# Kernel tuning notes

Hardware: AMD Instinct MI355X
Metric: run time of the kernel (lower is better)

The kernel has to match this reference:

```python
import jax, jax.numpy as jnp
import numpy as np

EPS = 1e-7
TAU = 2.0  # curr_temp = max_temp at init
GROUPS = 2
NUM_CODES = 320


def setup_inputs() -> dict:
    key = jax.random.key(0)
    k1, k2, k3, k4 = jax.random.split(key, 4)
    B, T, C = 8, 2048, 1024
    GV = GROUPS * NUM_CODES  # 640
    D = 256
    x = jax.random.normal(k1, (B, T, C), dtype=jnp.float32)
    W = jax.random.normal(k2, (GV, C), dtype=jnp.float32)  # nn.init.normal_(std=1)
    b = jnp.zeros((GV,), dtype=jnp.float32)
    codebook = jax.random.uniform(k3, (1, GV, D), dtype=jnp.float32)  # uniform_ init
    u = jax.random.uniform(k4, (B * T * GROUPS, NUM_CODES), dtype=jnp.float32,
                           minval=1e-10, maxval=1.0)
    gumbel_noise = -jnp.log(-jnp.log(u))
    return {"x": x, "W": W, "b": b, "codebook": codebook, "gumbel_noise": gumbel_noise}


def reference(x, W, b, codebook, gumbel_noise):
    B, T, C = x.shape
    N = B * T
    G, V = GROUPS, NUM_CODES
    D = codebook.shape[-1]

    # weight projection -> logits [N, G*V]
    logits = jnp.einsum('nc,vc->nv', x.reshape(N, C), W) + b
    l = logits.reshape(N * G, V)

    # hard codes (no-grad path in torch)
    k = jnp.argmax(l, axis=-1)
    hard_x = jax.nn.one_hot(k, V, dtype=l.dtype).reshape(N, G, V)
    hard_probs = jax.lax.stop_gradient(hard_x).mean(axis=0)  # [G, V]
    code_perplexity = jnp.exp(-jnp.sum(hard_probs * jnp.log(hard_probs + EPS), axis=-1)).sum()

    avg_probs = jax.nn.softmax(l.reshape(N, G, V), axis=-1).mean(axis=0)  # [G, V]
    prob_perplexity = jnp.exp(-jnp.sum(avg_probs * jnp.log(avg_probs + EPS), axis=-1)).sum()

    # gumbel-softmax, hard=True with straight-through (training path)
    y_soft = jax.nn.softmax((l + gumbel_noise) / TAU, axis=-1)  # [N*G, V]
    idx = jnp.argmax(y_soft, axis=-1)
    y_hard = jax.nn.one_hot(idx, V, dtype=y_soft.dtype)
    y = y_hard + y_soft - jax.lax.stop_gradient(y_soft)

    # combine with codebook: (onehot-ish weights) @ codebook per group
    q = jnp.einsum('ngv,gvd->ngd', y.reshape(N, G, V), codebook.reshape(G, V, D))
    q = q.reshape(B, T, G * D)

    num_vars = G * V
    diversity_loss = (num_vars - prob_perplexity) / num_vars
    return q, code_perplexity, prob_perplexity, diversity_loss
```

## Files before the change

kernel.cpp:

```cpp
#include <hip/hip_runtime.h>

#define N_ROWS 16384
#define C_DIM  1024
#define GV     640
#define V_DIM  320
#define G_DIM  2
#define D_DIM  256
#define MROWS  64
#define FBLKS  (N_ROWS / MROWS)
#define NBUCKET 64

typedef __attribute__((ext_vector_type(8))) _Float16 half8;
typedef __attribute__((ext_vector_type(4))) _Float16 half4v;
typedef __attribute__((ext_vector_type(4))) float float4v;

#define LDS_AS(p) ((__attribute__((address_space(3))) unsigned int*)(p))
#define GLB_AS(p) ((const __attribute__((address_space(1))) unsigned int*)(p))

__global__ __launch_bounds__(256) void wsplit_kernel(const float* __restrict__ src,
                                                     _Float16* __restrict__ dst,
                                                     int* __restrict__ zr) {
  const int t = blockIdx.x * 256 + threadIdx.x;
  zr[t] = 0;
  const int n = t % GV;
  const int cc = t / GV;
  const int k = cc * 8;
  const float4 v0 = *(const float4*)(src + (size_t)n * C_DIM + k);
  const float4 v1 = *(const float4*)(src + (size_t)n * C_DIM + k + 4);
  half8 h;
  h[0] = (_Float16)v0.x; h[1] = (_Float16)v0.y; h[2] = (_Float16)v0.z; h[3] = (_Float16)v0.w;
  h[4] = (_Float16)v1.x; h[5] = (_Float16)v1.y; h[6] = (_Float16)v1.z; h[7] = (_Float16)v1.w;
  *(half8*)(dst + (size_t)t * 8) = h;
}

__global__ __launch_bounds__(512, 2) void fused_kernel(
    const float* __restrict__ x,
    const _Float16* __restrict__ whT,
    const float* __restrict__ bias,
    const float* __restrict__ gn,
    const float* __restrict__ cb,
    float* __restrict__ q,
    float* __restrict__ mf,
    int* __restrict__ mi) {
  __shared__ __align__(16) char smemU[98304];
  _Float16* BhL = (_Float16*)smemU;
  _Float16* AhL = (_Float16*)(smemU + 81920);
  _Float16* AlL = (_Float16*)(smemU + 90112);
  float* combW  = (float*)smemU;
  float* wbL    = (float*)(smemU + 18432);
  __shared__ float accL[GV];
  __shared__ int   cntL[GV];

  const int tid = threadIdx.x;
  const int lane = tid & 63;
  const int w = tid >> 6;
  const int m0 = blockIdx.x * MROWS;
  const int frow = lane & 15;
  const int quad = lane >> 4;

  for (int e = tid; e < GV; e += 512) { accL[e] = 0.0f; cntL[e] = 0; }

  const int ar = tid >> 3;
  const int ak = (tid & 7) * 4;
  const int ac = ak >> 3;
  const int ah_off = ak & 7;
  const float* xp = x + (size_t)(m0 + ar) * C_DIM + ak;

  float4v acc[4][5];
#pragma unroll
  for (int i = 0; i < 4; ++i)
#pragma unroll
    for (int j = 0; j < 5; ++j) acc[i][j] = (float4v)0.0f;

  auto stageB = [&](int kb, _Float16* Bh) {
    const _Float16* bsrc = whT + (size_t)kb * 2560 * 8;
#pragma unroll
    for (int s = 0; s < 5; ++s) {
      const int c = s * 512 + tid;
      __builtin_amdgcn_global_load_lds(GLB_AS(bsrc + (size_t)c * 8),
                                       LDS_AS(Bh + c * 8), 16, 0, 0);
    }
  };
  auto splitA = [&](const float4& a4, _Float16* Ah, _Float16* Al) {
    const _Float16 h0 = (_Float16)a4.x, h1 = (_Float16)a4.y;
    const _Float16 h2 = (_Float16)a4.z, h3 = (_Float16)a4.w;
    half4v hv, lv;
    hv[0] = h0; hv[1] = h1; hv[2] = h2; hv[3] = h3;
    lv[0] = (_Float16)(a4.x - (float)h0);
    lv[1] = (_Float16)(a4.y - (float)h1);
    lv[2] = (_Float16)(a4.z - (float)h2);
    lv[3] = (_Float16)(a4.w - (float)h3);
    *(half4v*)&Ah[(ac * 64 + ar) * 8 + ah_off] = hv;
    *(half4v*)&Al[(ac * 64 + ar) * 8 + ah_off] = lv;
  };

  float4 a4 = *(const float4*)xp;
  stageB(0, BhL);
  splitA(a4, AhL, AlL);
  a4 = *(const float4*)(xp + 32);
  __syncthreads();

  for (int kb = 0; kb < 32; ++kb) {
    const int cur = kb & 1;
    _Float16* BhC = BhL + cur * 20480;
    _Float16* AhC = AhL + cur * 2048;
    _Float16* AlC = AlL + cur * 2048;

    if (kb < 31) {
      const int nxt = cur ^ 1;
      stageB(kb + 1, BhL + nxt * 20480);
      splitA(a4, AhL + nxt * 2048, AlL + nxt * 2048);
      if (kb < 30) a4 = *(const float4*)(xp + (kb + 2) * 32);
    }

    half8 ah[4], al[4];
#pragma unroll
    for (int i = 0; i < 4; ++i) {
      ah[i] = *(const half8*)&AhC[(quad * 64 + 16 * i + frow) * 8];
      al[i] = *(const half8*)&AlC[(quad * 64 + 16 * i + frow) * 8];
    }
#pragma unroll
    for (int j = 0; j < 5; ++j) {
      const half8 bh = *(const half8*)&BhC[(quad * 640 + 80 * w + 16 * j + frow) * 8];
#pragma unroll
      for (int i = 0; i < 4; ++i) {
        acc[i][j] = __builtin_amdgcn_mfma_f32_16x16x32_f16(ah[i], bh, acc[i][j], 0, 0, 0);
        acc[i][j] = __builtin_amdgcn_mfma_f32_16x16x32_f16(al[i], bh, acc[i][j], 0, 0, 0);
      }
    }
    __syncthreads();
  }

  float bw[5];
#pragma unroll
  for (int j = 0; j < 5; ++j) bw[j] = bias[80 * w + 16 * j + frow];

  const int g  = w >> 2;
  const int wq = w & 3;

  float mlk[4][4];
#pragma unroll
  for (int i = 0; i < 4; ++i) {
#pragma unroll
    for (int r = 0; r < 4; ++r) {
      const int row = 16 * i + 4 * quad + r;
      const int n = m0 + row;
      const float* gp = gn + (size_t)(2 * n + g) * V_DIM + 80 * wq + frow;

      float l5[5], t5[5];
#pragma unroll
      for (int j = 0; j < 5; ++j) {
        l5[j] = acc[i][j][r] + bw[j];
        t5[j] = (l5[j] + gp[16 * j]) * 0.5f;
      }
      float ml = l5[0]; int il = 80 * wq + frow;
      float mt = t5[0]; int it = il;
#pragma unroll
      for (int j = 1; j < 5; ++j) {
        const int cj = 80 * wq + 16 * j + frow;
        if (l5[j] > ml) { ml = l5[j]; il = cj; }
        if (t5[j] > mt) { mt = t5[j]; it = cj; }
      }
#pragma unroll
      for (int off = 1; off < 16; off <<= 1) {
        const float o1 = __shfl_xor(ml, off, 64); const int i1 = __shfl_xor(il, off, 64);
        if (o1 > ml || (o1 == ml && i1 < il)) { ml = o1; il = i1; }
        const float o2 = __shfl_xor(mt, off, 64); const int i2 = __shfl_xor(it, off, 64);
        if (o2 > mt || (o2 == mt && i2 < it)) { mt = o2; it = i2; }
      }
      mlk[i][r] = ml;
      float sl = 0.0f, st = 0.0f;
#pragma unroll
      for (int j = 0; j < 5; ++j) {
        const float el = expf(l5[j] - ml);
        acc[i][j][r] = el;
        sl += el;
        st += expf(t5[j] - mt);
      }
#pragma unroll
      for (int off = 1; off < 16; off <<= 1) {
        sl += __shfl_xor(sl, off, 64);
        st += __shfl_xor(st, off, 64);
      }
      if (frow == 4 * i + r) {
        float* dst = combW + (size_t)(g * 64 + row) * 36 + wq * 8;
        float4v p1, p2;
        p1[0] = ml; p1[1] = __int_as_float(il); p1[2] = sl; p1[3] = 0.0f;
        p2[0] = mt; p2[1] = __int_as_float(it); p2[2] = st; p2[3] = 0.0f;
        *(float4v*)dst = p1;
        *(float4v*)(dst + 4) = p2;
      }
    }
  }
  __syncthreads();

  if (tid < 128) {
    const int rg = tid;
    const float* cw = combW + (size_t)rg * 36;
    float mw[4], sw[4], tw[4], s2[4];
    int   iw[4], ti4[4];
#pragma unroll
    for (int v = 0; v < 4; ++v) {
      const float4v p1 = *(const float4v*)(cw + v * 8);
      const float4v p2 = *(const float4v*)(cw + v * 8 + 4);
      mw[v] = p1[0]; iw[v] = __float_as_int(p1[1]); sw[v] = p1[2];
      tw[v] = p2[0]; ti4[v] = __float_as_int(p2[1]); s2[v] = p2[2];
    }
    float m = mw[0]; int idx = iw[0];
    float tm = tw[0]; int ti = ti4[0];
#pragma unroll
    for (int v = 1; v < 4; ++v) {
      if (mw[v] > m || (mw[v] == m && iw[v] < idx)) { m = mw[v]; idx = iw[v]; }
      if (tw[v] > tm || (tw[v] == tm && ti4[v] < ti)) { tm = tw[v]; ti = ti4[v]; }
    }
    float sl = 0.0f, st = 0.0f;
#pragma unroll
    for (int v = 0; v < 4; ++v) {
      sl += sw[v] * expf(mw[v] - m);
      st += s2[v] * expf(tw[v] - tm);
    }
    const float inv = 1.0f / sl;
    const float sv = 1.0f / st;
    const float yv = (1.0f + sv) - sv;
    const int g2 = rg >> 6;
    atomicAdd(&cntL[g2 * V_DIM + idx], 1);
    float4v wbv;
    wbv[0] = m; wbv[1] = inv; wbv[2] = yv; wbv[3] = __int_as_float(ti);
    *(float4v*)(wbL + (size_t)rg * 4) = wbv;
  }
  __syncthreads();

  float p5[5] = {0.0f, 0.0f, 0.0f, 0.0f, 0.0f};
#pragma unroll
  for (int i = 0; i < 4; ++i)
#pragma unroll
    for (int r = 0; r < 4; ++r) {
      const int row = 16 * i + 4 * quad + r;
      const float4v wbv = *(const float4v*)(wbL + (size_t)(g * 64 + row) * 4);
      const float k = expf(mlk[i][r] - wbv[0]) * wbv[1];
#pragma unroll
      for (int j = 0; j < 5; ++j) p5[j] += acc[i][j][r] * k;
    }
#pragma unroll
  for (int j = 0; j < 5; ++j)
    atomicAdd(&accL[g * V_DIM + 80 * wq + 16 * j + frow], p5[j]);

#pragma unroll
  for (int it2 = 0; it2 < 16; ++it2) {
    const int task = w + 8 * it2;
    const int tg = task >> 6, trow = task & 63;
    const float4v wbv = *(const float4v*)(wbL + (size_t)task * 4);
    const float yv = wbv[2];
    const int ti = __float_as_int(wbv[3]);
    const float4v c4 = ((const float4v*)cb)[(size_t)(tg * V_DIM + ti) * 64 + lane];
    float4v o4;
#pragma unroll
    for (int e2 = 0; e2 < 4; ++e2) o4[e2] = yv * c4[e2];
    ((float4v*)q)[(size_t)(m0 + trow) * 128 + tg * 64 + lane] = o4;
  }

  __syncthreads();
  const size_t pb = (size_t)(blockIdx.x & (NBUCKET - 1)) * GV;
  for (int e = tid; e < GV; e += 512) {
    atomicAdd(&mf[pb + e], accL[e]);
    atomicAdd(&mi[pb + e], cntL[e]);
  }
}

__global__ __launch_bounds__(640) void finalize_kernel(
    const float* __restrict__ mf, const int* __restrict__ mi,
    float* __restrict__ out3) {
  __shared__ float sA[G_DIM];
  __shared__ float sC[G_DIM];
  const int t = threadIdx.x;
  if (t < G_DIM) { sA[t] = 0.0f; sC[t] = 0.0f; }
  __syncthreads();

  const int g = t / V_DIM;
  float f = 0.0f;
  int   c = 0;
#pragma unroll 8
  for (int b = 0; b < NBUCKET; ++b) {
    f += mf[(size_t)b * GV + t];
    c += mi[(size_t)b * GV + t];
  }
  const float pa = f * (1.0f / 16384.0f);
  const float ph = (float)c * (1.0f / 16384.0f);
  float a = pa * logf(pa + 1e-7f);
  float h = ph * logf(ph + 1e-7f);
#pragma unroll
  for (int off = 32; off > 0; off >>= 1) {
    a += __shfl_xor(a, off, 64);
    h += __shfl_xor(h, off, 64);
  }
  if ((t & 63) == 0) {
    atomicAdd(&sA[g], a);
    atomicAdd(&sC[g], h);
  }
  __syncthreads();
  if (t == 0) {
    const float code_p = expf(-sC[0]) + expf(-sC[1]);
    const float prob_p = expf(-sA[0]) + expf(-sA[1]);
    out3[0] = code_p;
    out3[1] = prob_p;
    out3[2] = ((float)GV - prob_p) / (float)GV;
  }
}

extern "C" void kernel_launch(void* const* d_in, const int* in_sizes, int n_in,
                              void* d_out, int out_size, void* d_ws, size_t ws_size,
                              hipStream_t stream) {
  const float* x  = (const float*)d_in[0];
  const float* W  = (const float*)d_in[1];
  const float* b  = (const float*)d_in[2];
  const float* cb = (const float*)d_in[3];
  const float* gn = (const float*)d_in[4];
  float* out = (float*)d_out;

  char* ws = (char*)d_ws;
  _Float16* whT = (_Float16*)ws;
  float* mf = (float*)(ws + 1310720);
  int*   mi = (int*)  (ws + 1474560);

  wsplit_kernel<<<(GV * C_DIM / 8) / 256, 256, 0, stream>>>(W, whT, (int*)mf);

  fused_kernel<<<FBLKS, 512, 0, stream>>>(x, whT, b, gn, cb, out, mf, mi);

  finalize_kernel<<<1, 640, 0, stream>>>(mf, mi, out + (size_t)N_ROWS * 512);
}
```

Baseline: 203.1 us.

## Halve row tile to 32 and drop double buffering for higher occupancy

The fused GEMM+softmax kernel now processes 32 rows per block instead of 64. It uses a single LDS buffer instead of double-buffered B and A tiles, which halves shared memory and registers so that four blocks per CU can be requested. The intent is to double the grid and hide latency through occupancy rather than software pipelining, since the kernel appears latency-bound. In exchange, each block reloads the full fp16 weight per k-step for half as many rows, which doubles L2 and LDS traffic for B, and loads are no longer overlapped with MFMA inside a block.

```diff
diff --git a/kernel.cpp b/kernel.cpp
--- a/kernel.cpp
+++ b/kernel.cpp
@@ -6,12 +6,12 @@
 #define V_DIM  320
 #define G_DIM  2
 #define D_DIM  256
-#define MROWS  64
+#define MROWS  32
 #define FBLKS  (N_ROWS / MROWS)
 #define NBUCKET 64
 
 typedef __attribute__((ext_vector_type(8))) _Float16 half8;
-typedef __attribute__((ext_vector_type(4))) _Float16 half4v;
+typedef __attribute__((ext_vector_type(2))) _Float16 half2v;
 typedef __attribute__((ext_vector_type(4))) float float4v;
 
 #define LDS_AS(p) ((__attribute__((address_space(3))) unsigned int*)(p))
@@ -33,7 +33,7 @@
   *(half8*)(dst + (size_t)t * 8) = h;
 }
 
-__global__ __launch_bounds__(512, 2) void fused_kernel(
+__global__ __launch_bounds__(512, 4) void fused_kernel(
     const float* __restrict__ x,
     const _Float16* __restrict__ whT,
     const float* __restrict__ bias,
@@ -42,12 +42,12 @@
     float* __restrict__ q,
     float* __restrict__ mf,
     int* __restrict__ mi) {
-  __shared__ __align__(16) char smemU[98304];
+  __shared__ __align__(16) char smemU[49152];
   _Float16* BhL = (_Float16*)smemU;
-  _Float16* AhL = (_Float16*)(smemU + 81920);
-  _Float16* AlL = (_Float16*)(smemU + 90112);
+  _Float16* AhL = (_Float16*)(smemU + 40960);
+  _Float16* AlL = (_Float16*)(smemU + 45056);
   float* combW  = (float*)smemU;
-  float* wbL    = (float*)(smemU + 18432);
+  float* wbL    = (float*)(smemU + 9216);
   __shared__ float accL[GV];
   __shared__ int   cntL[GV];
 
@@ -60,70 +60,49 @@
 
   for (int e = tid; e < GV; e += 512) { accL[e] = 0.0f; cntL[e] = 0; }
 
-  const int ar = tid >> 3;
-  const int ak = (tid & 7) * 4;
+  const int ar = tid >> 4;
+  const int ak = (tid & 15) * 2;
   const int ac = ak >> 3;
   const int ah_off = ak & 7;
   const float* xp = x + (size_t)(m0 + ar) * C_DIM + ak;
 
-  float4v acc[4][5];
-#pragma unroll
-  for (int i = 0; i < 4; ++i)
+  float4v acc[2][5];
+#pragma unroll
+  for (int i = 0; i < 2; ++i)
 #pragma unroll
     for (int j = 0; j < 5; ++j) acc[i][j] = (float4v)0.0f;
 
-  auto stageB = [&](int kb, _Float16* Bh) {
+  float2 a2 = *(const float2*)xp;
+
+  for (int kb = 0; kb < 32; ++kb) {
     const _Float16* bsrc = whT + (size_t)kb * 2560 * 8;
 #pragma unroll
     for (int s = 0; s < 5; ++s) {
       const int c = s * 512 + tid;
       __builtin_amdgcn_global_load_lds(GLB_AS(bsrc + (size_t)c * 8),
-                                       LDS_AS(Bh + c * 8), 16, 0, 0);
-    }
-  };
-  auto splitA = [&](const float4& a4, _Float16* Ah, _Float16* Al) {
-    const _Float16 h0 = (_Float16)a4.x, h1 = (_Float16)a4.y;
-    const _Float16 h2 = (_Float16)a4.z, h3 = (_Float16)a4.w;
-    half4v hv, lv;
-    hv[0] = h0; hv[1] = h1; hv[2] = h2; hv[3] = h3;
-    lv[0] = (_Float16)(a4.x - (float)h0);
-    lv[1] = (_Float16)(a4.y - (float)h1);
-    lv[2] = (_Float16)(a4.z - (float)h2);
-    lv[3] = (_Float16)(a4.w - (float)h3);
-    *(half4v*)&Ah[(ac * 64 + ar) * 8 + ah_off] = hv;
-    *(half4v*)&Al[(ac * 64 + ar) * 8 + ah_off] = lv;
-  };
-
-  float4 a4 = *(const float4*)xp;
-  stageB(0, BhL);
-  splitA(a4, AhL, AlL);
-  a4 = *(const float4*)(xp + 32);
-  __syncthreads();
-
-  for (int kb = 0; kb < 32; ++kb) {
-    const int cur = kb & 1;
-    _Float16* BhC = BhL + cur * 20480;
-    _Float16* AhC = AhL + cur * 2048;
-    _Float16* AlC = AlL + cur * 2048;
-
-    if (kb < 31) {
-      const int nxt = cur ^ 1;
-      stageB(kb + 1, BhL + nxt * 20480);
-      splitA(a4, AhL + nxt * 2048, AlL + nxt * 2048);
-      if (kb < 30) a4 = *(const float4*)(xp + (kb + 2) * 32);
-    }
-
-    half8 ah[4], al[4];
-#pragma unroll
-    for (int i = 0; i < 4; ++i) {
-      ah[i] = *(const half8*)&AhC[(quad * 64 + 16 * i + frow) * 8];
-      al[i] = *(const half8*)&AlC[(quad * 64 + 16 * i + frow) * 8];
+                                       LDS_AS(BhL + c * 8), 16, 0, 0);
+    }
+    const _Float16 h0 = (_Float16)a2.x, h1 = (_Float16)a2.y;
+    half2v hv, lv;
+    hv.x = h0; hv.y = h1;
+    lv.x = (_Float16)(a2.x - (float)h0);
+    lv.y = (_Float16)(a2.y - (float)h1);
+    *(half2v*)&AhL[(ac * 32 + ar) * 8 + ah_off] = hv;
+    *(half2v*)&AlL[(ac * 32 + ar) * 8 + ah_off] = lv;
+    if (kb < 31) a2 = *(const float2*)(xp + (kb + 1) * 32);
+    __syncthreads();
+
+    half8 ah[2], al[2];
+#pragma unroll
+    for (int i = 0; i < 2; ++i) {
+      ah[i] = *(const half8*)&AhL[(quad * 32 + 16 * i + frow) * 8];
+      al[i] = *(const half8*)&AlL[(quad * 32 + 16 * i + frow) * 8];
     }
 #pragma unroll
     for (int j = 0; j < 5; ++j) {
-      const half8 bh = *(const half8*)&BhC[(quad * 640 + 80 * w + 16 * j + frow) * 8];
-#pragma unroll
-      for (int i = 0; i < 4; ++i) {
+      const half8 bh = *(const half8*)&BhL[(quad * 640 + 80 * w + 16 * j + frow) * 8];
+#pragma unroll
+      for (int i = 0; i < 2; ++i) {
         acc[i][j] = __builtin_amdgcn_mfma_f32_16x16x32_f16(ah[i], bh, acc[i][j], 0, 0, 0);
         acc[i][j] = __builtin_amdgcn_mfma_f32_16x16x32_f16(al[i], bh, acc[i][j], 0, 0, 0);
       }
@@ -138,9 +117,9 @@
   const int g  = w >> 2;
   const int wq = w & 3;
 
-  float mlk[4][4];
-#pragma unroll
-  for (int i = 0; i < 4; ++i) {
+  float mlk[2][4];
+#pragma unroll
+  for (int i = 0; i < 2; ++i) {
 #pragma unroll
     for (int r = 0; r < 4; ++r) {
       const int row = 16 * i + 4 * quad + r;
@@ -183,7 +162,7 @@
         st += __shfl_xor(st, off, 64);
       }
       if (frow == 4 * i + r) {
-        float* dst = combW + (size_t)(g * 64 + row) * 36 + wq * 8;
+        float* dst = combW + (size_t)(g * 32 + row) * 36 + wq * 8;
         float4v p1, p2;
         p1[0] = ml; p1[1] = __int_as_float(il); p1[2] = sl; p1[3] = 0.0f;
         p2[0] = mt; p2[1] = __int_as_float(it); p2[2] = st; p2[3] = 0.0f;
@@ -194,7 +173,7 @@
   }
   __syncthreads();
 
-  if (tid < 128) {
+  if (tid < 64) {
     const int rg = tid;
     const float* cw = combW + (size_t)rg * 36;
     float mw[4], sw[4], tw[4], s2[4];
@@ -222,7 +201,7 @@
     const float inv = 1.0f / sl;
     const float sv = 1.0f / st;
     const float yv = (1.0f + sv) - sv;
-    const int g2 = rg >> 6;
+    const int g2 = rg >> 5;
     atomicAdd(&cntL[g2 * V_DIM + idx], 1);
     float4v wbv;
     wbv[0] = m; wbv[1] = inv; wbv[2] = yv; wbv[3] = __int_as_float(ti);
@@ -232,11 +211,11 @@
 
   float p5[5] = {0.0f, 0.0f, 0.0f, 0.0f, 0.0f};
 #pragma unroll
-  for (int i = 0; i < 4; ++i)
+  for (int i = 0; i < 2; ++i)
 #pragma unroll
     for (int r = 0; r < 4; ++r) {
       const int row = 16 * i + 4 * quad + r;
-      const float4v wbv = *(const float4v*)(wbL + (size_t)(g * 64 + row) * 4);
+      const float4v wbv = *(const float4v*)(wbL + (size_t)(g * 32 + row) * 4);
       const float k = expf(mlk[i][r] - wbv[0]) * wbv[1];
 #pragma unroll
       for (int j = 0; j < 5; ++j) p5[j] += acc[i][j][r] * k;
@@ -246,9 +225,9 @@
     atomicAdd(&accL[g * V_DIM + 80 * wq + 16 * j + frow], p5[j]);
 
 #pragma unroll
-  for (int it2 = 0; it2 < 16; ++it2) {
+  for (int it2 = 0; it2 < 8; ++it2) {
     const int task = w + 8 * it2;
-    const int tg = task >> 6, trow = task & 63;
+    const int tg = task >> 5, trow = task & 31;
     const float4v wbv = *(const float4v*)(wbL + (size_t)task * 4);
     const float yv = wbv[2];
     const int ti = __float_as_int(wbv[3]);
```

Result: no change. 206.5 us (+1.7%).
